# Performance work log

Hardware: AMD Instinct MI355X
Metric: run time of the kernel (lower is better)

Reference implementation:

```python
import jax, jax.numpy as jnp
import numpy as np

N = 100000      # nodes
E = 1600000     # edges
D = 128         # hidden_dim
H = 8           # num_heads
DH = D // H     # per-head dim (out_dim in MultiHeadAttentionLayer)
EPS = 1e-5


def layer_norm(x, g, b):
    mu = jnp.mean(x, axis=-1, keepdims=True)
    var = jnp.var(x, axis=-1, keepdims=True)
    return (x - mu) * jax.lax.rsqrt(var + EPS) * g + b


def setup_inputs() -> dict:
    key = jax.random.key(0)
    ks = jax.random.split(key, 16)
    s = 1.0 / np.sqrt(D)
    inp = {
        "h": jax.random.normal(ks[0], (N, D), jnp.float32),
        "src": jax.random.randint(ks[1], (E,), 0, N, jnp.int32),
        "dst": jax.random.randint(ks[2], (E,), 0, N, jnp.int32),
        # attention projections (use_bias=False)
        "Wq": jax.random.uniform(ks[3], (D, D), jnp.float32, -s, s),
        "Wk": jax.random.uniform(ks[4], (D, D), jnp.float32, -s, s),
        "Wv": jax.random.uniform(ks[5], (D, D), jnp.float32, -s, s),
        # output projection O (bias=True)
        "Wo": jax.random.uniform(ks[6], (D, D), jnp.float32, -s, s),
        "bo": jnp.zeros((D,), jnp.float32),
        # layer norms
        "g1": jnp.ones((D,), jnp.float32),
        "b1": jnp.zeros((D,), jnp.float32),
        "g2": jnp.ones((D,), jnp.float32),
        "b2": jnp.zeros((D,), jnp.float32),
        # FFN
        "W1": jax.random.uniform(ks[7], (D, 2 * D), jnp.float32, -s, s),
        "c1": jnp.zeros((2 * D,), jnp.float32),
        "W2": jax.random.uniform(ks[8], (2 * D, D), jnp.float32, -1.0 / np.sqrt(2 * D), 1.0 / np.sqrt(2 * D)),
        "c2": jnp.zeros((D,), jnp.float32),
    }
    return inp


def reference(h, src, dst, Wq, Wk, Wv, Wo, bo, g1, b1, g2, b2, W1, c1, W2, c2):
    n = h.shape[0]
    Q = (h @ Wq).reshape(n, H, DH)
    K = (h @ Wk).reshape(n, H, DH)
    V = (h @ Wv).reshape(n, H, DH)

    # per-edge score: (K[src] * Q[dst]).sum(-1), scaled exp with clamp
    score = jnp.einsum('ehd,ehd->eh', K[src], Q[dst])          # [E, H]
    score = jnp.exp(jnp.clip(score / np.sqrt(DH), -5.0, 5.0))  # [E, H]

    # scatter-sum aggregation into destination nodes
    wV = jax.ops.segment_sum(V[src] * score[:, :, None], dst, num_segments=n)  # [N, H, DH]
    z = jax.ops.segment_sum(score, dst, num_segments=n)                        # [N, H]

    # possible_empty=True: divide only where z > 0
    zb = z[:, :, None]
    head_out = jnp.where(zb > 0, wV / jnp.where(zb > 0, zb, 1.0), wV)

    a = head_out.reshape(n, D) @ Wo + bo
    hh = layer_norm(h + a, g1, b1)
    ff = jax.nn.relu(hh @ W1 + c1) @ W2 + c2
    return layer_norm(hh + ff, g2, b2)
```

## Files before the change

### kernel.cpp

```cpp
#include <hip/hip_runtime.h>
#include <hip/hip_bf16.h>

#define D 128
#define MAXB 512

typedef __attribute__((ext_vector_type(8))) short short8;
typedef __attribute__((ext_vector_type(4))) float float4v;
typedef __attribute__((ext_vector_type(2))) float float2v;

__device__ __forceinline__ float4v mfma16(short8 a, short8 b, float4v c) {
  return __builtin_amdgcn_mfma_f32_16x16x32_bf16(a, b, c, 0, 0, 0);
}
__device__ __forceinline__ float b2f(__hip_bfloat16 x) { return __bfloat162float(x); }
__device__ __forceinline__ __hip_bfloat16 f2b(float x) { return __float2bfloat16(x); }
__device__ __forceinline__ unsigned short f2b_bits(float x) {
  __hip_bfloat16 h = __float2bfloat16(x);
  return *reinterpret_cast<unsigned short*>(&h);
}

__device__ __forceinline__ float ldf(const float* p, size_t i) { return p[i]; }
__device__ __forceinline__ float ldf(const __hip_bfloat16* p, size_t i) { return b2f(p[i]); }
__device__ __forceinline__ void stf(float* p, size_t i, float v) { p[i] = v; }
__device__ __forceinline__ void stf(__hip_bfloat16* p, size_t i, float v) { p[i] = f2b(v); }

__device__ __forceinline__ void bar_lds() {
  asm volatile("s_waitcnt lgkmcnt(0)\n\ts_barrier" ::: "memory");
}

__device__ __forceinline__ float2v up2(unsigned w) {
  float2v r;
  r.x = __uint_as_float(w << 16);
  r.y = __uint_as_float(w & 0xffff0000u);
  return r;
}
__device__ __forceinline__ unsigned char f2fp8(float x) {
  int r = __builtin_amdgcn_cvt_pk_fp8_f32(x, x, 0, false);
  return (unsigned char)(r & 0xff);
}
__device__ __forceinline__ float2v cvt2lo(unsigned w) {
  return __builtin_amdgcn_cvt_pk_f32_fp8(w, false);
}
__device__ __forceinline__ float2v cvt2hi(unsigned w) {
  return __builtin_amdgcn_cvt_pk_f32_fp8(w, true);
}

__device__ __forceinline__ short8 cvt8(float4 u0, float4 u1) {
  short8 a;
  a[0] = (short)f2b_bits(u0.x); a[1] = (short)f2b_bits(u0.y);
  a[2] = (short)f2b_bits(u0.z); a[3] = (short)f2b_bits(u0.w);
  a[4] = (short)f2b_bits(u1.x); a[5] = (short)f2b_bits(u1.y);
  a[6] = (short)f2b_bits(u1.z); a[7] = (short)f2b_bits(u1.w);
  return a;
}

__global__ __launch_bounds__(256) void k_bhist_cast(
    const int* __restrict__ dst, int* __restrict__ bh, int E,
    const float* __restrict__ wq, const float* __restrict__ wk,
    const float* __restrict__ wv, const float* __restrict__ wo,
    const float* __restrict__ w1, const float* __restrict__ w2,
    __hip_bfloat16* __restrict__ oq, __hip_bfloat16* __restrict__ ok,
    __hip_bfloat16* __restrict__ ov, __hip_bfloat16* __restrict__ oo,
    __hip_bfloat16* __restrict__ o1, __hip_bfloat16* __restrict__ o2) {
  __shared__ int cnt[MAXB];
  const int t = threadIdx.x;
  const int gid = blockIdx.x * 256 + t;
  for (int i = t; i < MAXB; i += 256) cnt[i] = 0;
  __syncthreads();
  for (int e = gid; e < E; e += gridDim.x * 256) atomicAdd(&cnt[dst[e] >> 8], 1);
  int i = gid;
  if (i < 65536) {
    int m = i & 16383;
    int which = i >> 14;
    const float* s = (which == 0) ? wq : (which == 1) ? wk : (which == 2) ? wv : wo;
    __hip_bfloat16* o = (which == 0) ? oq : (which == 1) ? ok : (which == 2) ? ov : oo;
    int j = m & 7, t2 = m >> 3;
    int col = t2 & 127, cq = t2 >> 7;
    o[m] = f2b(s[((cq >> 2) * 32 + (cq & 3) * 8 + j) * 128 + col]);
  } else if (i < 98304) {
    int m = i - 65536;
    int j = m & 7, t2 = m >> 3;
    int col = t2 & 255, cq = t2 >> 8;
    o1[m] = f2b(w1[((cq >> 2) * 32 + (cq & 3) * 8 + j) * 256 + col]);
  } else if (i < 131072) {
    int m = i - 98304;
    int j = m & 7, t2 = m >> 3;
    int col = t2 & 127, cq = t2 >> 7;
    o2[m] = f2b(w2[((cq >> 2) * 32 + (cq & 3) * 8 + j) * 128 + col]);
  }
  __syncthreads();
  for (int k = t; k < MAXB; k += 256)
    if (cnt[k]) atomicAdd(&bh[k], cnt[k]);
}

__global__ void k_bscan(const int* __restrict__ bh, int* __restrict__ bbase,
                        int* __restrict__ bcur, int B) {
  __shared__ int sd[MAXB];
  int t = threadIdx.x;
  int v = (t < B) ? bh[t] : 0;
  sd[t] = v;
  __syncthreads();
  for (int o = 1; o < MAXB; o <<= 1) {
    int x = (t >= o) ? sd[t - o] : 0;
    __syncthreads();
    sd[t] += x;
    __syncthreads();
  }
  if (t < B) {
    int e = sd[t] - v;
    bbase[t] = e;
    bcur[t] = e;
  }
}

__global__ __launch_bounds__(256) void k_bin(const int* __restrict__ src,
                                             const int* __restrict__ dst,
                                             int* __restrict__ bcur,
                                             unsigned* __restrict__ binned, int E) {
  __shared__ int cnt[MAXB];
  __shared__ int base[MAXB];
  const int t = threadIdx.x;
  const int e0 = blockIdx.x * 4096;
  for (int i = t; i < MAXB; i += 256) cnt[i] = 0;
  __syncthreads();
  int myb[16], myr[16];
  unsigned pk[16];
#pragma unroll
  for (int j = 0; j < 16; ++j) {
    int e = e0 + j * 256 + t;
    if (e < E) {
      int d = dst[e];
      pk[j] = ((unsigned)src[e] << 8) | (unsigned)(d & 255);
      int b = d >> 8;
      myb[j] = b;
      myr[j] = atomicAdd(&cnt[b], 1);
    } else {
      myb[j] = -1;
    }
  }
  __syncthreads();
  for (int i = t; i < MAXB; i += 256)
    base[i] = cnt[i] ? atomicAdd(&bcur[i], cnt[i]) : 0;
  __syncthreads();
#pragma unroll
  for (int j = 0; j < 16; ++j)
    if (myb[j] >= 0) binned[(size_t)base[myb[j]] + myr[j]] = pk[j];
}

__global__ __launch_bounds__(256) void k_fine(const unsigned* __restrict__ binned,
                                              const int* __restrict__ bh,
                                              const int* __restrict__ bbase,
                                              int* __restrict__ deg,
                                              int* __restrict__ offs,
                                              int* __restrict__ csr, int N) {
  __shared__ int cnt[256];
  __shared__ int cur[256];
  __shared__ int sd[256];
  const int b = blockIdx.x, t = threadIdx.x;
  const int node0 = b << 8;
  cnt[t] = 0;
  __syncthreads();
  const int s0 = bbase[b], len = bh[b];
  for (int i = t; i < len; i += 256) atomicAdd(&cnt[binned[(size_t)s0 + i] & 255], 1);
  __syncthreads();
  int v = cnt[t];
  sd[t] = v;
  __syncthreads();
  for (int o = 1; o < 256; o <<= 1) {
    int x = (t >= o) ? sd[t - o] : 0;
    __syncthreads();
    sd[t] += x;
    __syncthreads();
  }
  int excl = sd[t] - v;
  cur[t] = excl;
  int node = node0 + t;
  if (node < N) {
    deg[node] = v;
    offs[node] = s0 + excl;
  }
  __syncthreads();
  for (int i = t; i < len; i += 256) {
    unsigned ed = binned[(size_t)s0 + i];
    int p = atomicAdd(&cur[ed & 255], 1);
    csr[s0 + p] = (int)(ed >> 8);
  }
}

__global__ __launch_bounds__(512, 2) void gemm_qkv8(const float* __restrict__ A,
                                                    const uint4* __restrict__ wqF,
                                                    const uint4* __restrict__ wkF,
                                                    const uint4* __restrict__ wvF,
                                                    __hip_bfloat16* __restrict__ Q,
                                                    unsigned char* __restrict__ KV8,
                                                    int Nrow) {
  __shared__ short W[3 * 16384];
  const int t = threadIdx.x;
  {
    uint4* W4 = (uint4*)W;
    for (int i = t; i < 2048; i += 512) {
      W4[i] = wqF[i];
      W4[i + 2048] = wkF[i];
      W4[i + 4096] = wvF[i];
    }
  }
  __syncthreads();
  const int w = t >> 6;
  const int lane = t & 63;
  const int n = lane & 15, quad = lane >> 4;
  const int ntiles = Nrow >> 4;
  const int step = gridDim.x * 8;
  int rt = blockIdx.x * 8 + w;
  if (rt >= ntiles) return;
  float4 u[8];
  {
    const float* Ap = A + (size_t)(rt * 16 + n) * 128 + quad * 8;
#pragma unroll
    for (int c = 0; c < 4; ++c) {
      u[2 * c] = *(const float4*)(Ap + c * 32);
      u[2 * c + 1] = *(const float4*)(Ap + c * 32 + 4);
    }
  }
  while (true) {
    const int rtn = rt + step;
    const bool more = rtn < ntiles;
    float4 un[8];
    if (more) {
      const float* Ap = A + (size_t)(rtn * 16 + n) * 128 + quad * 8;
#pragma unroll
      for (int c = 0; c < 4; ++c) {
        un[2 * c] = *(const float4*)(Ap + c * 32);
        un[2 * c + 1] = *(const float4*)(Ap + c * 32 + 4);
      }
    }
    short8 a[4];
#pragma unroll
    for (int c = 0; c < 4; ++c) a[c] = cvt8(u[2 * c], u[2 * c + 1]);
    float4v acc[8];
#pragma unroll
    for (int ct2 = 0; ct2 < 8; ++ct2) acc[ct2] = (float4v){0.f, 0.f, 0.f, 0.f};
#pragma unroll
    for (int c = 0; c < 4; ++c) {
      const int fb = ((c * 4 + quad) * 128 + n) * 8;
#pragma unroll
      for (int ct2 = 0; ct2 < 8; ++ct2)
        acc[ct2] = mfma16(a[c], *(const short8*)&W[fb + ct2 * 128], acc[ct2]);
    }
#pragma unroll
    for (int r = 0; r < 4; ++r) {
      const size_t qb = (size_t)(rt * 16 + quad * 4 + r) * 128 + n;
#pragma unroll
      for (int ct2 = 0; ct2 < 8; ++ct2) Q[qb + ct2 * 16] = f2b(acc[ct2][r]);
    }
#pragma unroll
    for (int ct2 = 0; ct2 < 8; ++ct2) acc[ct2] = (float4v){0.f, 0.f, 0.f, 0.f};
#pragma unroll
    for (int c = 0; c < 4; ++c) {
      const int fb = ((c * 4 + quad) * 128 + n) * 8;
#pragma unroll
      for (int ct2 = 0; ct2 < 8; ++ct2)
        acc[ct2] = mfma16(a[c], *(const short8*)&W[16384 + fb + ct2 * 128], acc[ct2]);
    }
#pragma unroll
    for (int r = 0; r < 4; ++r) {
      const size_t kb = (size_t)(rt * 16 + quad * 4 + r) * 256 + ((n >> 3) << 4) + (n & 7);
#pragma unroll
      for (int ct2 = 0; ct2 < 8; ++ct2) KV8[kb + ct2 * 32] = f2fp8(acc[ct2][r]);
    }
#pragma unroll
    for (int ct2 = 0; ct2 < 8; ++ct2) acc[ct2] = (float4v){0.f, 0.f, 0.f, 0.f};
#pragma unroll
    for (int c = 0; c < 4; ++c) {
      const int fb = ((c * 4 + quad) * 128 + n) * 8;
#pragma unroll
      for (int ct2 = 0; ct2 < 8; ++ct2)
        acc[ct2] = mfma16(a[c], *(const short8*)&W[32768 + fb + ct2 * 128], acc[ct2]);
    }
#pragma unroll
    for (int r = 0; r < 4; ++r) {
      const size_t kb = (size_t)(rt * 16 + quad * 4 + r) * 256 + ((n >> 3) << 4) + (n & 7);
#pragma unroll
      for (int ct2 = 0; ct2 < 8; ++ct2) KV8[kb + ct2 * 32 + 8] = f2fp8(acc[ct2][r]);
    }
    if (!more) break;
#pragma unroll
    for (int i = 0; i < 8; ++i) u[i] = un[i];
    rt = rtn;
  }
}

__global__ __launch_bounds__(512) void ln_gemm2(const short* __restrict__ A,
                                                const uint4* __restrict__ BF4,
                                                const float* __restrict__ bias,
                                                const float* __restrict__ resid,
                                                const float* __restrict__ gam,
                                                const float* __restrict__ bet,
                                                __hip_bfloat16* __restrict__ Out,
                                                int Nrow) {
  __shared__ short W[16384];
  const int t = threadIdx.x;
  {
    uint4* W4 = (uint4*)W;
    for (int i = t; i < 2048; i += 512) W4[i] = BF4[i];
  }
  __syncthreads();
  const int w = t >> 6;
  const int lane = t & 63;
  const int n = lane & 15, quad = lane >> 4;
  float gv[8], bv[8], biasv[8];
#pragma unroll
  for (int ct2 = 0; ct2 < 8; ++ct2) {
    gv[ct2] = gam[ct2 * 16 + n];
    bv[ct2] = bet[ct2 * 16 + n];
    biasv[ct2] = bias[ct2 * 16 + n];
  }
  const int ntiles = Nrow >> 4;
  for (int rt = blockIdx.x * 8 + w; rt < ntiles; rt += gridDim.x * 8) {
    const short8* Ap = (const short8*)(A + (size_t)(rt * 16 + n) * 128 + quad * 8);
    short8 a[4];
#pragma unroll
    for (int c = 0; c < 4; ++c) a[c] = Ap[c * 4];
    float4v acc[8];
#pragma unroll
    for (int ct2 = 0; ct2 < 8; ++ct2) acc[ct2] = (float4v){0.f, 0.f, 0.f, 0.f};
#pragma unroll
    for (int c = 0; c < 4; ++c) {
      const short8 af = a[c];
      const int fb = ((c * 4 + quad) * 128 + n) * 8;
#pragma unroll
      for (int ct2 = 0; ct2 < 8; ++ct2)
        acc[ct2] = mfma16(af, *(const short8*)&W[fb + ct2 * 128], acc[ct2]);
    }
#pragma unroll
    for (int r = 0; r < 4; ++r) {
      const size_t base = (size_t)(rt * 16 + quad * 4 + r) * 128 + n;
#pragma unroll
      for (int ct2 = 0; ct2 < 8; ++ct2)
        acc[ct2][r] += biasv[ct2] + resid[base + ct2 * 16];
    }
    float s[4] = {0.f, 0.f, 0.f, 0.f}, s2[4] = {0.f, 0.f, 0.f, 0.f};
#pragma unroll
    for (int ct2 = 0; ct2 < 8; ++ct2)
#pragma unroll
      for (int r = 0; r < 4; ++r) {
        float x = acc[ct2][r];
        s[r] += x;
        s2[r] += x * x;
      }
#pragma unroll
    for (int r = 0; r < 4; ++r)
#pragma unroll
      for (int o = 1; o <= 8; o <<= 1) {
        s[r] += __shfl_xor(s[r], o);
        s2[r] += __shfl_xor(s2[r], o);
      }
#pragma unroll
    for (int r = 0; r < 4; ++r) {
      float mean = s[r] * 0.0078125f;
      float var = s2[r] * 0.0078125f - mean * mean;
      float rstd = rsqrtf(var + 1e-5f);
      const size_t base = (size_t)(rt * 16 + quad * 4 + r) * 128 + n;
#pragma unroll
      for (int ct2 = 0; ct2 < 8; ++ct2)
        Out[base + ct2 * 16] = f2b((acc[ct2][r] - mean) * rstd * gv[ct2] + bv[ct2]);
    }
  }
}

__global__ __launch_bounds__(512) void ffn_ln(const short* __restrict__ hh,
                                              const uint4* __restrict__ W1F4,
                                              const float* __restrict__ c1,
                                              const uint4* __restrict__ W2F4,
                                              const float* __restrict__ c2,
                                              const float* __restrict__ gam,
                                              const float* __restrict__ bet,
                                              float* __restrict__ Out, int Nrow) {
  __shared__ short W1[32768];
  __shared__ short W2[32768];
  __shared__ short mid[2][16][264];
  __shared__ float tile[16][132];
  const int t = threadIdx.x;
  {
    uint4* a4 = (uint4*)W1;
    uint4* b4 = (uint4*)W2;
    for (int i = t; i < 4096; i += 512) {
      a4[i] = W1F4[i];
      b4[i] = W2F4[i];
    }
  }
  __syncthreads();
  const int lane = t & 63;
  const int wv = t >> 6;
  const int n = lane & 15, quad = lane >> 4;
  float b1v0 = c1[(wv * 2) * 16 + n], b1v1 = c1[(wv * 2 + 1) * 16 + n];
  float b2v = c2[wv * 16 + n];
  const int row2 = t >> 5, sub = t & 31;
  float ga0 = gam[sub],      ga1 = gam[sub + 32];
  float ga2 = gam[sub + 64], ga3 = gam[sub + 96];
  float be0 = bet[sub],      be1 = bet[sub + 32];
  float be2 = bet[sub + 64], be3 = bet[sub + 96];
  const int ntiles = Nrow >> 4;
  const __hip_bfloat16* hb = (const __hip_bfloat16*)hh;
  const int f1b0 = quad * 256 + (wv * 2) * 16 + n;
  const int f1b1 = quad * 256 + (wv * 2 + 1) * 16 + n;
  const int f2b = quad * 128 + wv * 16 + n;
  int rt = blockIdx.x;
  if (rt >= ntiles) return;
  short8 a[4];
  __hip_bfloat16 rs[4];
  {
    const short8* Ap = (const short8*)(hh + (size_t)(rt * 16 + n) * 128 + quad * 8);
#pragma unroll
    for (int c = 0; c < 4; ++c) a[c] = Ap[c * 4];
#pragma unroll
    for (int r = 0; r < 4; ++r)
      rs[r] = hb[(size_t)(rt * 16 + quad * 4 + r) * 128 + wv * 16 + n];
  }
  int mp = 0;
  while (true) {
    const int rtn = rt + gridDim.x;
    const bool more = rtn < ntiles;
    short8 an[4];
    __hip_bfloat16 rsn[4];
    if (more) {
      const short8* Ap = (const short8*)(hh + (size_t)(rtn * 16 + n) * 128 + quad * 8);
#pragma unroll
      for (int c = 0; c < 4; ++c) an[c] = Ap[c * 4];
#pragma unroll
      for (int r = 0; r < 4; ++r)
        rsn[r] = hb[(size_t)(rtn * 16 + quad * 4 + r) * 128 + wv * 16 + n];
    }
    float4v a10 = {0.f, 0.f, 0.f, 0.f}, a11 = a10;
#pragma unroll
    for (int c = 0; c < 4; ++c) {
      short8 f1a = *(const short8*)&W1[(f1b0 + c * 1024) * 8];
      short8 f1c = *(const short8*)&W1[(f1b1 + c * 1024) * 8];
      a10 = mfma16(a[c], f1a, a10);
      a11 = mfma16(a[c], f1c, a11);
    }
#pragma unroll
    for (int r = 0; r < 4; ++r) {
      mid[mp][quad * 4 + r][(wv * 2) * 16 + n] = (short)f2b_bits(fmaxf(a10[r] + b1v0, 0.f));
      mid[mp][quad * 4 + r][(wv * 2 + 1) * 16 + n] = (short)f2b_bits(fmaxf(a11[r] + b1v1, 0.f));
    }
    bar_lds();
    float4v acc = {0.f, 0.f, 0.f, 0.f};
#pragma unroll
    for (int c = 0; c < 8; ++c) {
      short8 am = *(const short8*)&mid[mp][n][quad * 8 + c * 32];
      short8 f2 = *(const short8*)&W2[(f2b + c * 512) * 8];
      acc = mfma16(am, f2, acc);
    }
#pragma unroll
    for (int r = 0; r < 4; ++r)
      tile[quad * 4 + r][wv * 16 + n] = acc[r] + b2v + b2f(rs[r]);
    bar_lds();
    float x0 = tile[row2][sub], x1 = tile[row2][sub + 32];
    float x2 = tile[row2][sub + 64], x3 = tile[row2][sub + 96];
    float s = x0 + x1 + x2 + x3;
    float s2 = x0 * x0 + x1 * x1 + x2 * x2 + x3 * x3;
#pragma unroll
    for (int o = 16; o >= 1; o >>= 1) {
      s += __shfl_xor(s, o);
      s2 += __shfl_xor(s2, o);
    }
    float mean = s * 0.0078125f;
    float var = s2 * 0.0078125f - mean * mean;
    float rstd = rsqrtf(var + 1e-5f);
    size_t base = (size_t)(rt * 16 + row2) * 128;
    Out[base + sub]      = (x0 - mean) * rstd * ga0 + be0;
    Out[base + sub + 32] = (x1 - mean) * rstd * ga1 + be1;
    Out[base + sub + 64] = (x2 - mean) * rstd * ga2 + be2;
    Out[base + sub + 96] = (x3 - mean) * rstd * ga3 + be3;
    if (!more) break;
#pragma unroll
    for (int c = 0; c < 4; ++c) a[c] = an[c];
#pragma unroll
    for (int r = 0; r < 4; ++r) rs[r] = rsn[r];
    rt = rtn;
    mp ^= 1;
  }
}

__global__ __launch_bounds__(256) void attn_agg5(const uint4* __restrict__ Q4,
                                                 const uint4* __restrict__ KV8,
                                                 const int* __restrict__ offs,
                                                 const int* __restrict__ deg,
                                                 const int* __restrict__ csr,
                                                 uint4* __restrict__ AT4, int N) {
  const int lane = threadIdx.x & 63;
  const int wv = threadIdx.x >> 6;
  const int e4 = lane >> 4;
  const int hd = (lane >> 1) & 7;
  const int hf = lane & 1;
  const int kvo = hd * 2 + hf;
  for (int node = blockIdx.x * 4 + wv; node < N; node += gridDim.x * 4) {
    uint4 qa = Q4[(size_t)node * 16 + kvo];
    float2v qv[4];
    qv[0] = up2(qa.x); qv[1] = up2(qa.y); qv[2] = up2(qa.z); qv[3] = up2(qa.w);
    float2v acc[4];
#pragma unroll
    for (int d = 0; d < 4; ++d) acc[d] = (float2v){0.f, 0.f};
    float z = 0.f;
    const int st = offs[node], dg = deg[node];
    if (dg > 0) {
      const int dgm1 = dg - 1;
      int s_cur = csr[st + min(e4, dgm1)];
      int s_nxt = (dg > 4) ? csr[st + min(4 + e4, dgm1)] : s_cur;
      uint4 ckv = KV8[(size_t)s_cur * 16 + kvo];
      int i = 0;
      while (true) {
        const bool more = (i + 4) < dg;
        uint4 nkv;
        int s_fut = s_nxt;
        if (more) {
          nkv = KV8[(size_t)s_nxt * 16 + kvo];
          s_fut = csr[st + min(i + 8 + e4, dgm1)];
        }
        float2v p2 = cvt2lo(ckv.x) * qv[0];
        p2 += cvt2hi(ckv.x) * qv[1];
        p2 += cvt2lo(ckv.y) * qv[2];
        p2 += cvt2hi(ckv.y) * qv[3];
        float p = p2.x + p2.y;
        p += __shfl_xor(p, 1);
        float sc = __expf(fminf(fmaxf(p * 0.25f, -5.f), 5.f));
        sc = ((i + e4) < dg) ? sc : 0.f;
        z += sc;
        float2v sv = {sc, sc};
        acc[0] += cvt2lo(ckv.z) * sv;
        acc[1] += cvt2hi(ckv.z) * sv;
        acc[2] += cvt2lo(ckv.w) * sv;
        acc[3] += cvt2hi(ckv.w) * sv;
        if (!more) break;
        ckv = nkv;
        s_nxt = s_fut;
        i += 4;
      }
    }
#pragma unroll
    for (int m = 16; m <= 32; m <<= 1) {
      z += __shfl_xor(z, m);
#pragma unroll
      for (int d = 0; d < 4; ++d) {
        acc[d].x += __shfl_xor(acc[d].x, m);
        acc[d].y += __shfl_xor(acc[d].y, m);
      }
    }
    if (e4 == 0) {
      float inv = (z > 0.f) ? 1.f / z : 1.f;
      unsigned r[4];
#pragma unroll
      for (int j = 0; j < 4; ++j)
        r[j] = (unsigned)f2b_bits(acc[j].x * inv) |
               ((unsigned)f2b_bits(acc[j].y * inv) << 16);
      AT4[(size_t)node * 16 + kvo] = make_uint4(r[0], r[1], r[2], r[3]);
    }
  }
}

extern "C" void kernel_launch(void* const* d_in, const int* in_sizes, int n_in,
                              void* d_out, int out_size, void* d_ws, size_t ws_size,
                              hipStream_t stream) {
  const float* h = (const float*)d_in[0];
  const int* src = (const int*)d_in[1];
  const int* dst = (const int*)d_in[2];
  const float* Wq = (const float*)d_in[3];
  const float* Wk = (const float*)d_in[4];
  const float* Wv = (const float*)d_in[5];
  const float* Wo = (const float*)d_in[6];
  const float* bo = (const float*)d_in[7];
  const float* g1 = (const float*)d_in[8];
  const float* b1 = (const float*)d_in[9];
  const float* g2 = (const float*)d_in[10];
  const float* b2 = (const float*)d_in[11];
  const float* W1 = (const float*)d_in[12];
  const float* c1 = (const float*)d_in[13];
  const float* W2 = (const float*)d_in[14];
  const float* c2 = (const float*)d_in[15];

  const int N = in_sizes[0] / D;
  const int E = in_sizes[1];
  const int B = (N + 255) >> 8;
  const int ntiles = N >> 4;

  char* p = (char*)d_ws;
  auto carve = [&](size_t bytes) {
    char* r = p;
    p += (bytes + 255) & ~(size_t)255;
    return r;
  };
  short* ATb = (short*)carve((size_t)N * D * 2);
  short* Qb = (short*)carve((size_t)N * D * 2);
  unsigned char* KVb = (unsigned char*)carve((size_t)N * 256);
  short* wq = (short*)carve(16384 * 2);
  short* wk = (short*)carve(16384 * 2);
  short* wv = (short*)carve(16384 * 2);
  short* wo = (short*)carve(16384 * 2);
  short* w1 = (short*)carve(32768 * 2);
  short* w2 = (short*)carve(32768 * 2);
  int* deg = (int*)carve((size_t)N * 4);
  int* offs = (int*)carve((size_t)N * 4);
  int* bh = (int*)carve(MAXB * 4);
  int* bbase = (int*)carve(MAXB * 4);
  int* bcur = (int*)carve(MAXB * 4);
  unsigned* binned = (unsigned*)carve((size_t)E * 4);
  int* csr = (int*)carve((size_t)E * 4);
  short* hh = Qb;

  hipMemsetAsync(bh, 0, MAXB * 4, stream);
  k_bhist_cast<<<1024, 256, 0, stream>>>(
      dst, bh, E, Wq, Wk, Wv, Wo, W1, W2,
      (__hip_bfloat16*)wq, (__hip_bfloat16*)wk, (__hip_bfloat16*)wv,
      (__hip_bfloat16*)wo, (__hip_bfloat16*)w1, (__hip_bfloat16*)w2);
  k_bscan<<<1, MAXB, 0, stream>>>(bh, bbase, bcur, B);
  k_bin<<<(E + 4095) / 4096, 256, 0, stream>>>(src, dst, bcur, binned, E);
  k_fine<<<B, 256, 0, stream>>>(binned, bh, bbase, deg, offs, csr, N);

  gemm_qkv8<<<256, 512, 0, stream>>>(h, (const uint4*)wq, (const uint4*)wk,
                                     (const uint4*)wv, (__hip_bfloat16*)Qb, KVb, N);

  attn_agg5<<<(N + 3) >> 2, 256, 0, stream>>>((const uint4*)Qb, (const uint4*)KVb,
                                              offs, deg, csr, (uint4*)ATb, N);

  ln_gemm2<<<(ntiles + 7) / 8, 512, 0, stream>>>(
      ATb, (const uint4*)wo, bo, h, g1, b1, (__hip_bfloat16*)hh, N);
  ffn_ln<<<256, 512, 0, stream>>>(hh, (const uint4*)w1, c1, (const uint4*)w2, c2,
                                  g2, b2, (float*)d_out, N);
}
```

Measured before the change: 356.1 us.

## Split fused FFN+LayerNorm into two barrier-free per-wave MFMA kernels

Replaces the single ffn_ln kernel, which kept both W1 and W2 in LDS and staged the intermediate through shared memory with block barriers, with two kernels. ffn_a computes relu(hh@W1+c1) into a global bf16 buffer. ffn_b computes the W2 GEMM, adds the residual, and applies the LayerNorm entirely in registers using shuffles. Each wave owns a 16-row tile, so no barriers are needed, and each kernel holds only one weight matrix in LDS, which frees LDS for higher occupancy. The cost is an extra round trip of the N×256 intermediate through global memory. That intermediate is written over the ATb buffer and runs past its end into the now-dead KV buffer, which is why the workspace ordering was swapped.

```diff
diff --git a/kernel.cpp b/kernel.cpp
--- a/kernel.cpp
+++ b/kernel.cpp
@@ -20,12 +20,6 @@
 
 __device__ __forceinline__ float ldf(const float* p, size_t i) { return p[i]; }
 __device__ __forceinline__ float ldf(const __hip_bfloat16* p, size_t i) { return b2f(p[i]); }
-__device__ __forceinline__ void stf(float* p, size_t i, float v) { p[i] = v; }
-__device__ __forceinline__ void stf(__hip_bfloat16* p, size_t i, float v) { p[i] = f2b(v); }
-
-__device__ __forceinline__ void bar_lds() {
-  asm volatile("s_waitcnt lgkmcnt(0)\n\ts_barrier" ::: "memory");
-}
 
 __device__ __forceinline__ float2v up2(unsigned w) {
   float2v r;
@@ -366,118 +360,130 @@
   }
 }
 
-__global__ __launch_bounds__(512) void ffn_ln(const short* __restrict__ hh,
-                                              const uint4* __restrict__ W1F4,
-                                              const float* __restrict__ c1,
-                                              const uint4* __restrict__ W2F4,
-                                              const float* __restrict__ c2,
-                                              const float* __restrict__ gam,
-                                              const float* __restrict__ bet,
-                                              float* __restrict__ Out, int Nrow) {
-  __shared__ short W1[32768];
-  __shared__ short W2[32768];
-  __shared__ short mid[2][16][264];
-  __shared__ float tile[16][132];
+__global__ __launch_bounds__(512) void ffn_a(const short* __restrict__ hh,
+                                             const uint4* __restrict__ W1F4,
+                                             const float* __restrict__ c1,
+                                             __hip_bfloat16* __restrict__ mid,
+                                             int Nrow) {
+  __shared__ short W[32768];
   const int t = threadIdx.x;
   {
-    uint4* a4 = (uint4*)W1;
-    uint4* b4 = (uint4*)W2;
-    for (int i = t; i < 4096; i += 512) {
-      a4[i] = W1F4[i];
-      b4[i] = W2F4[i];
-    }
-  }
-  __syncthreads();
+    uint4* W4 = (uint4*)W;
+    for (int i = t; i < 4096; i += 512) W4[i] = W1F4[i];
+  }
+  __syncthreads();
+  const int w = t >> 6;
   const int lane = t & 63;
-  const int wv = t >> 6;
   const int n = lane & 15, quad = lane >> 4;
-  float b1v0 = c1[(wv * 2) * 16 + n], b1v1 = c1[(wv * 2 + 1) * 16 + n];
-  float b2v = c2[wv * 16 + n];
-  const int row2 = t >> 5, sub = t & 31;
-  float ga0 = gam[sub],      ga1 = gam[sub + 32];
-  float ga2 = gam[sub + 64], ga3 = gam[sub + 96];
-  float be0 = bet[sub],      be1 = bet[sub + 32];
-  float be2 = bet[sub + 64], be3 = bet[sub + 96];
+  float c1v[2][8];
+#pragma unroll
+  for (int half = 0; half < 2; ++half)
+#pragma unroll
+    for (int ct2 = 0; ct2 < 8; ++ct2) c1v[half][ct2] = c1[half * 128 + ct2 * 16 + n];
   const int ntiles = Nrow >> 4;
+  for (int rt = blockIdx.x * 8 + w; rt < ntiles; rt += gridDim.x * 8) {
+    const short8* Ap = (const short8*)(hh + (size_t)(rt * 16 + n) * 128 + quad * 8);
+    short8 a[4];
+#pragma unroll
+    for (int c = 0; c < 4; ++c) a[c] = Ap[c * 4];
+    float4v acc[8];
+#pragma unroll
+    for (int half = 0; half < 2; ++half) {
+#pragma unroll
+      for (int ct2 = 0; ct2 < 8; ++ct2) acc[ct2] = (float4v){0.f, 0.f, 0.f, 0.f};
+#pragma unroll
+      for (int c = 0; c < 4; ++c) {
+        const int fb = ((c * 4 + quad) * 256 + half * 128 + n) * 8;
+#pragma unroll
+        for (int ct2 = 0; ct2 < 8; ++ct2)
+          acc[ct2] = mfma16(a[c], *(const short8*)&W[fb + ct2 * 128], acc[ct2]);
+      }
+#pragma unroll
+      for (int r = 0; r < 4; ++r) {
+        const size_t base = (size_t)(rt * 16 + quad * 4 + r) * 256 + half * 128 + n;
+#pragma unroll
+        for (int ct2 = 0; ct2 < 8; ++ct2)
+          mid[base + ct2 * 16] = f2b(fmaxf(acc[ct2][r] + c1v[half][ct2], 0.f));
+      }
+    }
+  }
+}
+
+__global__ __launch_bounds__(512) void ffn_b(const short* __restrict__ hh,
+                                             const short* __restrict__ midb,
+                                             const uint4* __restrict__ W2F4,
+                                             const float* __restrict__ c2,
+                                             const float* __restrict__ gam,
+                                             const float* __restrict__ bet,
+                                             float* __restrict__ Out, int Nrow) {
+  __shared__ short W[32768];
+  const int t = threadIdx.x;
+  {
+    uint4* W4 = (uint4*)W;
+    for (int i = t; i < 4096; i += 512) W4[i] = W2F4[i];
+  }
+  __syncthreads();
+  const int w = t >> 6;
+  const int lane = t & 63;
+  const int n = lane & 15, quad = lane >> 4;
   const __hip_bfloat16* hb = (const __hip_bfloat16*)hh;
-  const int f1b0 = quad * 256 + (wv * 2) * 16 + n;
-  const int f1b1 = quad * 256 + (wv * 2 + 1) * 16 + n;
-  const int f2b = quad * 128 + wv * 16 + n;
-  int rt = blockIdx.x;
-  if (rt >= ntiles) return;
-  short8 a[4];
-  __hip_bfloat16 rs[4];
-  {
-    const short8* Ap = (const short8*)(hh + (size_t)(rt * 16 + n) * 128 + quad * 8);
-#pragma unroll
-    for (int c = 0; c < 4; ++c) a[c] = Ap[c * 4];
+  float gv[8], bv[8], c2v[8];
+#pragma unroll
+  for (int ct2 = 0; ct2 < 8; ++ct2) {
+    gv[ct2] = gam[ct2 * 16 + n];
+    bv[ct2] = bet[ct2 * 16 + n];
+    c2v[ct2] = c2[ct2 * 16 + n];
+  }
+  const int ntiles = Nrow >> 4;
+  for (int rt = blockIdx.x * 8 + w; rt < ntiles; rt += gridDim.x * 8) {
+    const short8* Mp = (const short8*)(midb + (size_t)(rt * 16 + n) * 256 + quad * 8);
+    short8 a[8];
+#pragma unroll
+    for (int c = 0; c < 8; ++c) a[c] = Mp[c * 4];
+    float4v acc[8];
+#pragma unroll
+    for (int ct2 = 0; ct2 < 8; ++ct2) acc[ct2] = (float4v){0.f, 0.f, 0.f, 0.f};
+#pragma unroll
+    for (int c = 0; c < 8; ++c) {
+      const short8 af = a[c];
+      const int fb = ((c * 4 + quad) * 128 + n) * 8;
+#pragma unroll
+      for (int ct2 = 0; ct2 < 8; ++ct2)
+        acc[ct2] = mfma16(af, *(const short8*)&W[fb + ct2 * 128], acc[ct2]);
+    }
+#pragma unroll
+    for (int r = 0; r < 4; ++r) {
+      const size_t base = (size_t)(rt * 16 + quad * 4 + r) * 128 + n;
+#pragma unroll
+      for (int ct2 = 0; ct2 < 8; ++ct2)
+        acc[ct2][r] += c2v[ct2] + b2f(hb[base + ct2 * 16]);
+    }
+    float s[4] = {0.f, 0.f, 0.f, 0.f}, s2[4] = {0.f, 0.f, 0.f, 0.f};
+#pragma unroll
+    for (int ct2 = 0; ct2 < 8; ++ct2)
+#pragma unroll
+      for (int r = 0; r < 4; ++r) {
+        float x = acc[ct2][r];
+        s[r] += x;
+        s2[r] += x * x;
+      }
 #pragma unroll
     for (int r = 0; r < 4; ++r)
-      rs[r] = hb[(size_t)(rt * 16 + quad * 4 + r) * 128 + wv * 16 + n];
-  }
-  int mp = 0;
-  while (true) {
-    const int rtn = rt + gridDim.x;
-    const bool more = rtn < ntiles;
-    short8 an[4];
-    __hip_bfloat16 rsn[4];
-    if (more) {
-      const short8* Ap = (const short8*)(hh + (size_t)(rtn * 16 + n) * 128 + quad * 8);
-#pragma unroll
-      for (int c = 0; c < 4; ++c) an[c] = Ap[c * 4];
-#pragma unroll
-      for (int r = 0; r < 4; ++r)
-        rsn[r] = hb[(size_t)(rtn * 16 + quad * 4 + r) * 128 + wv * 16 + n];
-    }
-    float4v a10 = {0.f, 0.f, 0.f, 0.f}, a11 = a10;
-#pragma unroll
-    for (int c = 0; c < 4; ++c) {
-      short8 f1a = *(const short8*)&W1[(f1b0 + c * 1024) * 8];
-      short8 f1c = *(const short8*)&W1[(f1b1 + c * 1024) * 8];
-      a10 = mfma16(a[c], f1a, a10);
-      a11 = mfma16(a[c], f1c, a11);
-    }
+#pragma unroll
+      for (int o = 1; o <= 8; o <<= 1) {
+        s[r] += __shfl_xor(s[r], o);
+        s2[r] += __shfl_xor(s2[r], o);
+      }
 #pragma unroll
     for (int r = 0; r < 4; ++r) {
-      mid[mp][quad * 4 + r][(wv * 2) * 16 + n] = (short)f2b_bits(fmaxf(a10[r] + b1v0, 0.f));
-      mid[mp][quad * 4 + r][(wv * 2 + 1) * 16 + n] = (short)f2b_bits(fmaxf(a11[r] + b1v1, 0.f));
-    }
-    bar_lds();
-    float4v acc = {0.f, 0.f, 0.f, 0.f};
-#pragma unroll
-    for (int c = 0; c < 8; ++c) {
-      short8 am = *(const short8*)&mid[mp][n][quad * 8 + c * 32];
-      short8 f2 = *(const short8*)&W2[(f2b + c * 512) * 8];
-      acc = mfma16(am, f2, acc);
-    }
-#pragma unroll
-    for (int r = 0; r < 4; ++r)
-      tile[quad * 4 + r][wv * 16 + n] = acc[r] + b2v + b2f(rs[r]);
-    bar_lds();
-    float x0 = tile[row2][sub], x1 = tile[row2][sub + 32];
-    float x2 = tile[row2][sub + 64], x3 = tile[row2][sub + 96];
-    float s = x0 + x1 + x2 + x3;
-    float s2 = x0 * x0 + x1 * x1 + x2 * x2 + x3 * x3;
-#pragma unroll
-    for (int o = 16; o >= 1; o >>= 1) {
-      s += __shfl_xor(s, o);
-      s2 += __shfl_xor(s2, o);
-    }
-    float mean = s * 0.0078125f;
-    float var = s2 * 0.0078125f - mean * mean;
-    float rstd = rsqrtf(var + 1e-5f);
-    size_t base = (size_t)(rt * 16 + row2) * 128;
-    Out[base + sub]      = (x0 - mean) * rstd * ga0 + be0;
-    Out[base + sub + 32] = (x1 - mean) * rstd * ga1 + be1;
-    Out[base + sub + 64] = (x2 - mean) * rstd * ga2 + be2;
-    Out[base + sub + 96] = (x3 - mean) * rstd * ga3 + be3;
-    if (!more) break;
-#pragma unroll
-    for (int c = 0; c < 4; ++c) a[c] = an[c];
-#pragma unroll
-    for (int r = 0; r < 4; ++r) rs[r] = rsn[r];
-    rt = rtn;
-    mp ^= 1;
+      float mean = s[r] * 0.0078125f;
+      float var = s2[r] * 0.0078125f - mean * mean;
+      float rstd = rsqrtf(var + 1e-5f);
+      const size_t base = (size_t)(rt * 16 + quad * 4 + r) * 128 + n;
+#pragma unroll
+      for (int ct2 = 0; ct2 < 8; ++ct2)
+        Out[base + ct2 * 16] = (acc[ct2][r] - mean) * rstd * gv[ct2] + bv[ct2];
+    }
   }
 }
 
@@ -588,8 +594,8 @@
     p += (bytes + 255) & ~(size_t)255;
     return r;
   };
+  short* Qb = (short*)carve((size_t)N * D * 2);
   short* ATb = (short*)carve((size_t)N * D * 2);
-  short* Qb = (short*)carve((size_t)N * D * 2);
   unsigned char* KVb = (unsigned char*)carve((size_t)N * 256);
   short* wq = (short*)carve(16384 * 2);
   short* wk = (short*)carve(16384 * 2);
@@ -605,6 +611,7 @@
   unsigned* binned = (unsigned*)carve((size_t)E * 4);
   int* csr = (int*)carve((size_t)E * 4);
   short* hh = Qb;
+  short* midb = ATb;
 
   hipMemsetAsync(bh, 0, MAXB * 4, stream);
   k_bhist_cast<<<1024, 256, 0, stream>>>(
@@ -623,6 +630,9 @@
 
   ln_gemm2<<<(ntiles + 7) / 8, 512, 0, stream>>>(
       ATb, (const uint4*)wo, bo, h, g1, b1, (__hip_bfloat16*)hh, N);
-  ffn_ln<<<256, 512, 0, stream>>>(hh, (const uint4*)w1, c1, (const uint4*)w2, c2,
-                                  g2, b2, (float*)d_out, N);
-}
+
+  ffn_a<<<(ntiles + 7) / 8, 512, 0, stream>>>(hh, (const uint4*)w1, c1,
+                                              (__hip_bfloat16*)midb, N);
+  ffn_b<<<(ntiles + 7) / 8, 512, 0, stream>>>(hh, midb, (const uint4*)w2, c2,
+                                              g2, b2, (float*)d_out, N);
+}
```

New measurement: 482.0 us. +35.4%, slower.
